# Optimization experiments

Measured on AMD Instinct MI355X. Metric: run time of the kernel, lower is better.

Reference implementation:

```python
import jax, jax.numpy as jnp
import numpy as np

B, CIN, COUT, L = 16, 128, 128, 4096  # kernel_size == L required by the broadcast in the source
STRIDE, DIL, PAD = 1, 1, 0


def setup_inputs() -> dict:
    key = jax.random.key(0)
    kx, kw, kb = jax.random.split(key, 3)
    x = jax.random.normal(kx, (B, CIN, L), dtype=jnp.float32)
    # source does weight.data.int() then .float() in forward -> integer-truncated randn
    weight = jnp.trunc(jax.random.normal(kw, (COUT, CIN, L), dtype=jnp.float32))
    bias = jax.random.normal(kb, (COUT,), dtype=jnp.float32)
    return {"x": x, "weight": weight, "bias": bias}


def reference(x, weight, bias):
    # padding=0 -> F.pad is a no-op; output_size = (L + 2*0 - 1*(K-1) - 1)//1 + 1 = 1
    out_size = (L + 2 * PAD - DIL * (L - 1) - 1) // STRIDE + 1  # == 1
    x_f = jnp.fft.fft(x, axis=2)            # [B, Cin, L] complex64
    w_f = jnp.fft.fft(weight, axis=2)       # [Cout, Cin, L] complex64
    # faithful math of (x_f[:,None] * w_f[None]).sum(dim=2), expressed as a
    # per-frequency complex contraction to avoid the O(B*Cout*Cin*L) intermediate
    out_f = jnp.einsum('bil,oil->bol', x_f, w_f)  # [B, Cout, L]
    out = jnp.fft.ifft(out_f, axis=2).real
    out = out + bias[None, :, None]
    return out[:, :, :out_size]
```

## Files before the change

### kernel.cpp

```cpp
#include <hip/hip_runtime.h>


constexpr int LEN   = 4096;
constexpr int CIN_  = 128;
constexpr int COUT_ = 128;
constexpr int BATCH = 16;

typedef float f32x4 __attribute__((ext_vector_type(4)));

__global__ void init_out_kernel(const float* __restrict__ bias, float* __restrict__ out) {
    int t = blockIdx.x * 256 + threadIdx.x;
    if (t < BATCH * COUT_) out[t] = bias[t & (COUT_ - 1)];
}

__device__ __forceinline__ f32x4 ntload4(const float* p) {
    return __builtin_nontemporal_load((const f32x4*)p);
}

__device__ __forceinline__ void gload_lds4(const float* g, float* l) {
    __builtin_amdgcn_global_load_lds(
        (const __attribute__((address_space(1))) unsigned int*)g,
        (__attribute__((address_space(3))) unsigned int*)l, 4, 0, 0);
}

__device__ __forceinline__ float quad_sum(float v) {
    v += __int_as_float(__builtin_amdgcn_update_dpp(
            0, __float_as_int(v), 0xB1, 0xF, 0xF, true));
    v += __int_as_float(__builtin_amdgcn_update_dpp(
            0, __float_as_int(v), 0x4E, 0xF, 0xF, true));
    return v;
}

__global__ __launch_bounds__(256, 2)
void conv_partial_kernel(const float* __restrict__ x, const float* __restrict__ w,
                         float* __restrict__ ws) {
    __shared__ float xls[8192];
    __shared__ float fl[4096];

    const int tid  = threadIdx.x;
    const int lane = tid & 63;
    const int wv   = __builtin_amdgcn_readfirstlane(tid >> 6);
    const int bk   = blockIdx.x;
    const int ms   = bk >> 7;
    const int ci   = bk & 127;
    const int m0   = ms << 9;

#pragma unroll
    for (int bb = 0; bb < 4; ++bb) {
        const int b = 4 * wv + bb;
        const float* xc = x + ((b * CIN_ + ci) << 12);
        float* dst = xls + (b << 9);
#pragma unroll
        for (int t = 0; t < 8; ++t) {
            const int n = (LEN - m0 - (t << 6) - lane) & (LEN - 1);
            gload_lds4(xc + n, dst + (t << 6));
        }
    }
    f32x4 wc[8];
#pragma unroll
    for (int j = 0; j < 4; ++j) {
        const float* wr = w + ((((wv * 4 + j) << 7) + ci) << 12) + m0;
        wc[j]     = ntload4(wr + (lane << 2));
        wc[4 + j] = ntload4(wr + 256 + (lane << 2));
    }
    __syncthreads();

    float acc[16][4];
#pragma unroll
    for (int b = 0; b < 16; ++b)
#pragma unroll
        for (int j = 0; j < 4; ++j) acc[b][j] = 0.f;

    const float4* xls4 = (const float4*)xls;
    float* fr  = fl + (wv << 10);
    float* wsb = ws + (size_t)bk * 2048;
    const int q  = lane >> 2;
    const int jo = lane & 3;

#pragma unroll 1
    for (int u = 0; u < 8; ++u) {
#pragma unroll
        for (int b = 0; b < 16; ++b) {
            const float4 xv0 = xls4[(b << 7) + lane];
            const float4 xv1 = xls4[(b << 7) + 64 + lane];
#pragma unroll
            for (int j = 0; j < 4; ++j) {
                acc[b][j] += xv0.x * wc[j].x + xv0.y * wc[j].y
                           + xv0.z * wc[j].z + xv0.w * wc[j].w;
                acc[b][j] += xv1.x * wc[4 + j].x + xv1.y * wc[4 + j].y
                           + xv1.z * wc[4 + j].z + xv1.w * wc[4 + j].w;
            }
        }
        if (u < 7) {
            const int row = (u + 1) * 16 + wv * 4;
#pragma unroll
            for (int j = 0; j < 4; ++j) {
                const float* wr = w + ((((row + j) << 7) + ci) << 12) + m0;
                wc[j]     = ntload4(wr + (lane << 2));
                wc[4 + j] = ntload4(wr + 256 + (lane << 2));
            }
        }
        __builtin_amdgcn_sched_barrier(0);
#pragma unroll
        for (int b = 0; b < 16; ++b) {
            const float qs0 = quad_sum(acc[b][0]);
            const float qs1 = quad_sum(acc[b][1]);
            const float qs2 = quad_sum(acc[b][2]);
            const float qs3 = quad_sum(acc[b][3]);
            const float v = (jo == 0) ? qs0 : (jo == 1) ? qs1
                          : (jo == 2) ? qs2 : qs3;
            fr[(b << 6) + ((q ^ b) << 2) + jo] = v;
            acc[b][0] = 0.f; acc[b][1] = 0.f; acc[b][2] = 0.f; acc[b][3] = 0.f;
        }
        {
            float s = 0.f;
#pragma unroll
            for (int k = 0; k < 16; ++k)
                s += fr[(q << 6) + ((k ^ q) << 2) + jo];
            wsb[(q << 7) + u * 16 + wv * 4 + jo] = s;
        }
    }
}

__global__ __launch_bounds__(256, 4)
void reduce_ws_kernel(const float* __restrict__ ws, float* __restrict__ out) {
    const int bo = ((blockIdx.x & 7) << 8) + threadIdx.x;
    const int s0 = (blockIdx.x >> 3) << 7;
    const float* p = ws + (size_t)s0 * 2048 + bo;
    float s = 0.f;
#pragma unroll 8
    for (int i = 0; i < 128; ++i) s += p[(size_t)i * 2048];
    atomicAdd(out + bo, s);
}

extern "C" void kernel_launch(void* const* d_in, const int* in_sizes, int n_in,
                              void* d_out, int out_size, void* d_ws, size_t ws_size,
                              hipStream_t stream) {
    const float* x    = (const float*)d_in[0];
    const float* wgt  = (const float*)d_in[1];
    const float* bias = (const float*)d_in[2];
    float* out = (float*)d_out;
    float* ws  = (float*)d_ws;
    (void)in_sizes; (void)n_in; (void)ws_size; (void)out_size;

    init_out_kernel<<<8, 256, 0, stream>>>(bias, out);
    conv_partial_kernel<<<1024, 256, 0, stream>>>(x, wgt, ws);
    reduce_ws_kernel<<<64, 256, 0, stream>>>(ws, out);
}
```

Measured before the change: 383.9 us.

## Stage weight tiles through triple-buffered LDS with async global_load_lds prefetch

Weight rows are no longer loaded into registers with nontemporal loads. They are now streamed into a three-slot LDS ring buffer using global_load_lds, two stages ahead of use, with manual vmcnt waits and barriers. The goal is deeper prefetch so HBM weight traffic overlaps the FMA and reduction work without holding the prefetched weights in VGPRs. In exchange, LDS use rises sharply (about 96KB extra per block), which may cut occupancy below the 2 blocks/CU target, and the hand-tuned vmcnt counts are fragile.

Result: slower. 445.7 us (+16.1%).

```diff
diff --git a/kernel.cpp b/kernel.cpp
--- a/kernel.cpp
+++ b/kernel.cpp
@@ -11,10 +11,6 @@
 __global__ void init_out_kernel(const float* __restrict__ bias, float* __restrict__ out) {
     int t = blockIdx.x * 256 + threadIdx.x;
     if (t < BATCH * COUT_) out[t] = bias[t & (COUT_ - 1)];
-}
-
-__device__ __forceinline__ f32x4 ntload4(const float* p) {
-    return __builtin_nontemporal_load((const f32x4*)p);
 }
 
 __device__ __forceinline__ void gload_lds4(const float* g, float* l) {
@@ -31,10 +27,24 @@
     return v;
 }
 
+#define WSTAGE(U, BUF)                                                        \
+    {                                                                         \
+        _Pragma("unroll")                                                     \
+        for (int rr = 0; rr < 4; ++rr) {                                      \
+            const int row = ((U) << 4) + 4 * wv + rr;                         \
+            const float* src = w + (((row << 7) + ci) << 12) + m0;            \
+            float* dst = wls + ((BUF) << 13) + ((4 * wv + rr) << 9);          \
+            _Pragma("unroll")                                                 \
+            for (int t = 0; t < 8; ++t)                                       \
+                gload_lds4(src + (t << 6) + lane, dst + (t << 6));            \
+        }                                                                     \
+    }
+
 __global__ __launch_bounds__(256, 2)
 void conv_partial_kernel(const float* __restrict__ x, const float* __restrict__ w,
                          float* __restrict__ ws) {
     __shared__ float xls[8192];
+    __shared__ float wls[3 * 8192];
     __shared__ float fl[4096];
 
     const int tid  = threadIdx.x;
@@ -56,14 +66,14 @@
             gload_lds4(xc + n, dst + (t << 6));
         }
     }
-    f32x4 wc[8];
-#pragma unroll
-    for (int j = 0; j < 4; ++j) {
-        const float* wr = w + ((((wv * 4 + j) << 7) + ci) << 12) + m0;
-        wc[j]     = ntload4(wr + (lane << 2));
-        wc[4 + j] = ntload4(wr + 256 + (lane << 2));
-    }
-    __syncthreads();
+    __builtin_amdgcn_sched_barrier(0);
+    WSTAGE(0, 0)
+    __builtin_amdgcn_sched_barrier(0);
+    WSTAGE(1, 1)
+    __builtin_amdgcn_sched_barrier(0);
+    asm volatile("s_waitcnt vmcnt(32)" ::: "memory");
+    __builtin_amdgcn_s_barrier();
+    __builtin_amdgcn_sched_barrier(0);
 
     float acc[16][4];
 #pragma unroll
@@ -79,28 +89,29 @@
 
 #pragma unroll 1
     for (int u = 0; u < 8; ++u) {
+        if (u < 6) WSTAGE(u + 2, (u + 2) % 3)
+        __builtin_amdgcn_sched_barrier(0);
+
+        const f32x4* wb4 = (const f32x4*)(wls + ((u % 3) << 13));
+        f32x4 wcv[8];
+#pragma unroll
+        for (int j = 0; j < 4; ++j) {
+            wcv[j]     = wb4[((4 * wv + j) << 7) + lane];
+            wcv[4 + j] = wb4[((4 * wv + j) << 7) + 64 + lane];
+        }
 #pragma unroll
         for (int b = 0; b < 16; ++b) {
             const float4 xv0 = xls4[(b << 7) + lane];
             const float4 xv1 = xls4[(b << 7) + 64 + lane];
 #pragma unroll
             for (int j = 0; j < 4; ++j) {
-                acc[b][j] += xv0.x * wc[j].x + xv0.y * wc[j].y
-                           + xv0.z * wc[j].z + xv0.w * wc[j].w;
-                acc[b][j] += xv1.x * wc[4 + j].x + xv1.y * wc[4 + j].y
-                           + xv1.z * wc[4 + j].z + xv1.w * wc[4 + j].w;
+                acc[b][j] += xv0.x * wcv[j].x + xv0.y * wcv[j].y
+                           + xv0.z * wcv[j].z + xv0.w * wcv[j].w;
+                acc[b][j] += xv1.x * wcv[4 + j].x + xv1.y * wcv[4 + j].y
+                           + xv1.z * wcv[4 + j].z + xv1.w * wcv[4 + j].w;
             }
         }
-        if (u < 7) {
-            const int row = (u + 1) * 16 + wv * 4;
-#pragma unroll
-            for (int j = 0; j < 4; ++j) {
-                const float* wr = w + ((((row + j) << 7) + ci) << 12) + m0;
-                wc[j]     = ntload4(wr + (lane << 2));
-                wc[4 + j] = ntload4(wr + 256 + (lane << 2));
-            }
-        }
-        __builtin_amdgcn_sched_barrier(0);
+
 #pragma unroll
         for (int b = 0; b < 16; ++b) {
             const float qs0 = quad_sum(acc[b][0]);
@@ -118,6 +129,16 @@
             for (int k = 0; k < 16; ++k)
                 s += fr[(q << 6) + ((k ^ q) << 2) + jo];
             wsb[(q << 7) + u * 16 + wv * 4 + jo] = s;
+        }
+
+        if (u < 6) {
+            asm volatile("s_waitcnt vmcnt(33)" ::: "memory");
+            __builtin_amdgcn_s_barrier();
+            __builtin_amdgcn_sched_barrier(0);
+        } else if (u == 6) {
+            asm volatile("s_waitcnt vmcnt(1)" ::: "memory");
+            __builtin_amdgcn_s_barrier();
+            __builtin_amdgcn_sched_barrier(0);
         }
     }
 }
```

## Use 512-thread blocks with double-buffered weight prefetch in conv partial kernel

Applied to the files above, without the earlier changes.

Doubles the block to 8 waves, so each wave handles 2 output channels per unit instead of 4. Weight registers are double-buffered so the load for unit u+2 is issued while unit u+1's weights are already resident. The full unit sequence is unrolled with scheduling barriers. This aims to hide weight-load latency and raise in-flight memory requests. The cost is more threads per block and tighter per-thread register budgets under the new launch bounds.

After: 401.2 us. 1.05x slower.

```diff
diff --git a/kernel.cpp b/kernel.cpp
--- a/kernel.cpp
+++ b/kernel.cpp
@@ -31,7 +31,53 @@
     return v;
 }
 
-__global__ __launch_bounds__(256, 2)
+#define WLOAD(WC, U)                                                          \
+    {                                                                         \
+        const float* wr_ = w + ((((16 * (U) + 2 * wv) << 7) + ci) << 12) + m0;\
+        WC[0] = ntload4(wr_ + lo);                                            \
+        WC[1] = ntload4(wr_ + 256 + lo);                                      \
+        WC[2] = ntload4(wr_ + (1 << 19) + lo);                \
+        WC[3] = ntload4(wr_ + (1 << 19) + 256 + lo);                          \
+    }
+
+#define UNIT(U, WC, ISSUE)                                                    \
+    {                                                                         \
+        __builtin_amdgcn_sched_barrier(0);                                    \
+        _Pragma("unroll")                                                     \
+        for (int b = 0; b < 16; ++b) {                                        \
+            const float4 xv0 = xls4[(b << 7) + lane];                         \
+            const float4 xv1 = xls4[(b << 7) + 64 + lane];                    \
+            acc[b][0] += xv0.x * WC[0].x + xv0.y * WC[0].y                    \
+                       + xv0.z * WC[0].z + xv0.w * WC[0].w;                   \
+            acc[b][0] += xv1.x * WC[1].x + xv1.y * WC[1].y                    \
+                       + xv1.z * WC[1].z + xv1.w * WC[1].w;                   \
+            acc[b][1] += xv0.x * WC[2].x + xv0.y * WC[2].y                    \
+                       + xv0.z * WC[2].z + xv0.w * WC[2].w;                   \
+            acc[b][1] += xv1.x * WC[3].x + xv1.y * WC[3].y                    \
+                       + xv1.z * WC[3].z + xv1.w * WC[3].w;                   \
+        }                                                                     \
+        __builtin_amdgcn_sched_barrier(0);                                    \
+        if (ISSUE) WLOAD(WC, (U) + 2)                                         \
+        __builtin_amdgcn_sched_barrier(0);                                    \
+        _Pragma("unroll")                                                     \
+        for (int b = 0; b < 16; ++b) {                                        \
+            const float qs0 = quad_sum(acc[b][0]);                            \
+            const float qs1 = quad_sum(acc[b][1]);                            \
+            if (jo < 2)                                                       \
+                fr[(b << 5) + ((q ^ b) << 1) + jo] = (jo == 0) ? qs0 : qs1;   \
+            acc[b][0] = 0.f; acc[b][1] = 0.f;                                 \
+        }                                                                     \
+        if (lane < 32) {                                                      \
+            const int b_ = lane >> 1, j_ = lane & 1;                          \
+            float s = 0.f;                                                    \
+            _Pragma("unroll")                                                 \
+            for (int k = 0; k < 16; ++k)                                      \
+                s += fr[(b_ << 5) + ((k ^ b_) << 1) + j_];                    \
+            wsb[(b_ << 7) + 16 * (U) + 2 * wv + j_] = s;                      \
+        }                                                                     \
+    }
+
+__global__ __launch_bounds__(512, 2)
 void conv_partial_kernel(const float* __restrict__ x, const float* __restrict__ w,
                          float* __restrict__ ws) {
     __shared__ float xls[8192];
@@ -44,10 +90,11 @@
     const int ms   = bk >> 7;
     const int ci   = bk & 127;
     const int m0   = ms << 9;
+    const int lo   = lane << 2;
 
 #pragma unroll
-    for (int bb = 0; bb < 4; ++bb) {
-        const int b = 4 * wv + bb;
+    for (int bb = 0; bb < 2; ++bb) {
+        const int b = 2 * wv + bb;
         const float* xc = x + ((b * CIN_ + ci) << 12);
         float* dst = xls + (b << 9);
 #pragma unroll
@@ -56,70 +103,31 @@
             gload_lds4(xc + n, dst + (t << 6));
         }
     }
-    f32x4 wc[8];
-#pragma unroll
-    for (int j = 0; j < 4; ++j) {
-        const float* wr = w + ((((wv * 4 + j) << 7) + ci) << 12) + m0;
-        wc[j]     = ntload4(wr + (lane << 2));
-        wc[4 + j] = ntload4(wr + 256 + (lane << 2));
-    }
+    __builtin_amdgcn_sched_barrier(0);
+
+    f32x4 wcA[4], wcB[4];
+    WLOAD(wcA, 0)
+    WLOAD(wcB, 1)
     __syncthreads();
 
-    float acc[16][4];
+    float acc[16][2];
 #pragma unroll
-    for (int b = 0; b < 16; ++b)
-#pragma unroll
-        for (int j = 0; j < 4; ++j) acc[b][j] = 0.f;
+    for (int b = 0; b < 16; ++b) { acc[b][0] = 0.f; acc[b][1] = 0.f; }
 
     const float4* xls4 = (const float4*)xls;
-    float* fr  = fl + (wv << 10);
+    float* fr  = fl + (wv << 9);
     float* wsb = ws + (size_t)bk * 2048;
     const int q  = lane >> 2;
     const int jo = lane & 3;
 
-#pragma unroll 1
-    for (int u = 0; u < 8; ++u) {
-#pragma unroll
-        for (int b = 0; b < 16; ++b) {
-            const float4 xv0 = xls4[(b << 7) + lane];
-            const float4 xv1 = xls4[(b << 7) + 64 + lane];
-#pragma unroll
-            for (int j = 0; j < 4; ++j) {
-                acc[b][j] += xv0.x * wc[j].x + xv0.y * wc[j].y
-                           + xv0.z * wc[j].z + xv0.w * wc[j].w;
-                acc[b][j] += xv1.x * wc[4 + j].x + xv1.y * wc[4 + j].y
-                           + xv1.z * wc[4 + j].z + xv1.w * wc[4 + j].w;
-            }
-        }
-        if (u < 7) {
-            const int row = (u + 1) * 16 + wv * 4;
-#pragma unroll
-            for (int j = 0; j < 4; ++j) {
-                const float* wr = w + ((((row + j) << 7) + ci) << 12) + m0;
-                wc[j]     = ntload4(wr + (lane << 2));
-                wc[4 + j] = ntload4(wr + 256 + (lane << 2));
-            }
-        }
-        __builtin_amdgcn_sched_barrier(0);
-#pragma unroll
-        for (int b = 0; b < 16; ++b) {
-            const float qs0 = quad_sum(acc[b][0]);
-            const float qs1 = quad_sum(acc[b][1]);
-            const float qs2 = quad_sum(acc[b][2]);
-            const float qs3 = quad_sum(acc[b][3]);
-            const float v = (jo == 0) ? qs0 : (jo == 1) ? qs1
-                          : (jo == 2) ? qs2 : qs3;
-            fr[(b << 6) + ((q ^ b) << 2) + jo] = v;
-            acc[b][0] = 0.f; acc[b][1] = 0.f; acc[b][2] = 0.f; acc[b][3] = 0.f;
-        }
-        {
-            float s = 0.f;
-#pragma unroll
-            for (int k = 0; k < 16; ++k)
-                s += fr[(q << 6) + ((k ^ q) << 2) + jo];
-            wsb[(q << 7) + u * 16 + wv * 4 + jo] = s;
-        }
-    }
+    UNIT(0, wcA, 1)
+    UNIT(1, wcB, 1)
+    UNIT(2, wcA, 1)
+    UNIT(3, wcB, 1)
+    UNIT(4, wcA, 1)
+    UNIT(5, wcB, 1)
+    UNIT(6, wcA, 0)
+    UNIT(7, wcB, 0)
 }
 
 __global__ __launch_bounds__(256, 4)
@@ -144,6 +152,6 @@
     (void)in_sizes; (void)n_in; (void)ws_size; (void)out_size;
 
     init_out_kernel<<<8, 256, 0, stream>>>(bias, out);
-    conv_partial_kernel<<<1024, 256, 0, stream>>>(x, wgt, ws);
+    conv_partial_kernel<<<1024, 512, 0, stream>>>(x, wgt, ws);
     reduce_ws_kernel<<<64, 256, 0, stream>>>(ws, out);
 }
```
